# Optimization experiments

Measured on AMD Instinct MI355X. Metric: run time of the kernel, lower is better.

Reference implementation:

```python
import jax, jax.numpy as jnp
import numpy as np
import math

B, T, C, H = 8, 1024, 1024, 16
HS = C // H  # head size 64
FF = 4 * C
EPS = 1e-5


def quant_weight(W, e, b):
    """Fake-quant with straight-through rounding, per QLinear.forward.
    W:[...,out,in], e:[...,out,1], b:[...,out,1] -> effective weight 2**e * round_ste(clip(2**-e * W))."""
    b_rel = jax.nn.relu(b)
    mn = jnp.where(b_rel > 0, -(2.0 ** (b_rel - 1)), 0.0)
    mx = jnp.where(b_rel > 0, 2.0 ** (b_rel - 1) - 1.0, 0.0)
    qw = jnp.clip((2.0 ** (-e)) * W, mn, mx)
    w = qw + jax.lax.stop_gradient(jnp.round(qw) - qw)  # STE round
    return (2.0 ** e) * w


def layer_norm(x, g, beta):
    mu = jnp.mean(x, axis=-1, keepdims=True)
    var = jnp.mean((x - mu) ** 2, axis=-1, keepdims=True)
    return (x - mu) * jax.lax.rsqrt(var + EPS) * g + beta


def _uniform(key, shape, fan_in):
    s = 1.0 / math.sqrt(fan_in)
    return jax.random.uniform(key, shape, jnp.float32, -s, s)


def setup_inputs() -> dict:
    key = jax.random.key(0)
    ks = jax.random.split(key, 8)
    d = {"x": jax.random.normal(ks[0], (B, T, C), jnp.float32)}
    # stacked per-head QKV QLinear params (bias=False)
    d["Wq"] = _uniform(ks[1], (H, HS, C), C)
    d["Wk"] = _uniform(ks[2], (H, HS, C), C)
    d["Wv"] = _uniform(ks[3], (H, HS, C), C)
    for n in ("q", "k", "v"):
        d["e" + n] = jnp.full((H, HS, 1), -8.0, jnp.float32)
        d["b" + n] = jnp.full((H, HS, 1), 32.0, jnp.float32)
    # output projection QLinear (bias=True)
    d["Wp"] = _uniform(ks[4], (C, C), C)
    d["ep"] = jnp.full((C, 1), -8.0, jnp.float32)
    d["bp"] = jnp.full((C, 1), 32.0, jnp.float32)
    d["biasp"] = jnp.zeros((C,), jnp.float32)
    # FFN QLinears
    d["W1"] = _uniform(ks[5], (FF, C), C)
    d["e1"] = jnp.full((FF, 1), -8.0, jnp.float32)
    d["b1"] = jnp.full((FF, 1), 32.0, jnp.float32)
    d["bias1"] = jnp.zeros((FF,), jnp.float32)
    d["W2"] = _uniform(ks[6], (C, FF), FF)
    d["e2"] = jnp.full((C, 1), -8.0, jnp.float32)
    d["b2"] = jnp.full((C, 1), 32.0, jnp.float32)
    d["bias2"] = jnp.zeros((C,), jnp.float32)
    # LayerNorms
    d["g1"] = jnp.ones((C,), jnp.float32)
    d["be1"] = jnp.zeros((C,), jnp.float32)
    d["g2"] = jnp.ones((C,), jnp.float32)
    d["be2"] = jnp.zeros((C,), jnp.float32)
    return d


def block_forward(x, Wq, eq, bq, Wk, ek, bk, Wv, ev, bv,
                  Wp, ep, bp, biasp, W1, e1, b1, bias1, W2, e2, b2, bias2,
                  g1, be1, g2, be2):
    h = layer_norm(x, g1, be1)
    q = jnp.einsum('btc,hdc->bhtd', h, quant_weight(Wq, eq, bq))
    k = jnp.einsum('btc,hdc->bhtd', h, quant_weight(Wk, ek, bk))
    v = jnp.einsum('btc,hdc->bhtd', h, quant_weight(Wv, ev, bv))
    # NOTE: source scales by C**-0.5 where C = n_embd (not head_size)
    wei = jnp.einsum('bhtd,bhsd->bhts', q, k) * (C ** -0.5)
    causal = jnp.tril(jnp.ones((T, T), bool))
    wei = jnp.where(causal, wei, -jnp.inf)
    wei = jax.nn.softmax(wei, axis=-1)
    att = jnp.einsum('bhts,bhsd->bhtd', wei, v)  # [B,H,T,HS]
    att = att.transpose(0, 2, 1, 3).reshape(B, T, C)  # concat heads
    x = x + att @ quant_weight(Wp, ep, bp).T + biasp
    h2 = layer_norm(x, g2, be2)
    f = jax.nn.relu(h2 @ quant_weight(W1, e1, b1).T + bias1)
    f = f @ quant_weight(W2, e2, b2).T + bias2
    return x + f


def reference(x, Wq, eq, bq, Wk, ek, bk, Wv, ev, bv,
              Wp, ep, bp, biasp, W1, e1, b1, bias1, W2, e2, b2, bias2,
              g1, be1, g2, be2):
    return block_forward(x, Wq, eq, bq, Wk, ek, bk, Wv, ev, bv,
                         Wp, ep, bp, biasp, W1, e1, b1, bias1, W2, e2, b2, bias2,
                         g1, be1, g2, be2)
```

## Files before the change

### kernel.cpp

```cpp
#include <hip/hip_runtime.h>
#include <hip/hip_bf16.h>
#include <math.h>

#define DEVI __device__ __forceinline__

typedef __attribute__((ext_vector_type(8))) short bf16x8;
typedef __attribute__((ext_vector_type(4))) float f32x4;

DEVI unsigned short f2bf(float f) {
    union { float f; unsigned u; } v; v.f = f;
    unsigned r = v.u + 0x7FFFu + ((v.u >> 16) & 1u);
    return (unsigned short)(r >> 16);
}

DEVI float bf2f(unsigned short u) {
    union { unsigned u; float f; } v; v.u = (unsigned)u << 16; return v.f;
}

DEVI unsigned cvtpk(float lo, float hi) {
    unsigned d;
    asm volatile("v_cvt_pk_bf16_f32 %0, %1, %2" : "=v"(d) : "v"(lo), "v"(hi));
    return d;
}

DEVI void gload16(const void* g, void* l) {
    __builtin_amdgcn_global_load_lds((const __attribute__((address_space(1))) void*)g,
                                     (__attribute__((address_space(3))) void*)l, 16, 0, 0);
}

#define WAITVM4() asm volatile("s_waitcnt vmcnt(4)" ::: "memory")
#define WAITVM0() asm volatile("s_waitcnt vmcnt(0)" ::: "memory")
#define WAITLG0() asm volatile("s_waitcnt lgkmcnt(0)" ::: "memory")
#define WAITLG8() asm volatile("s_waitcnt lgkmcnt(8)" ::: "memory")
#define BAR()     __builtin_amdgcn_s_barrier()
#define SB()      __builtin_amdgcn_sched_barrier(0)

__global__ __launch_bounds__(256) void fused_pre_kernel(
    const float* __restrict__ Wq, const float* __restrict__ Wk, const float* __restrict__ Wv,
    const float* __restrict__ Wp, const float* __restrict__ W1, const float* __restrict__ W2,
    const float* __restrict__ eq, const float* __restrict__ ek, const float* __restrict__ ev,
    const float* __restrict__ ep, const float* __restrict__ e1, const float* __restrict__ e2,
    const float* __restrict__ bq, const float* __restrict__ bk, const float* __restrict__ bv,
    const float* __restrict__ bp, const float* __restrict__ b1, const float* __restrict__ b2,
    unsigned short* __restrict__ Wqkvq, unsigned short* __restrict__ Wpq,
    unsigned short* __restrict__ W1q, unsigned short* __restrict__ W2q,
    const float* __restrict__ x, const float* __restrict__ g1, const float* __restrict__ be1,
    unsigned short* __restrict__ hbuf)
{
    const int M1 = 1 << 20;
    if (blockIdx.x < 2048) {
        const int NCH = 3 * M1;
        const int STRIDE = 2048 * 256;
        for (int c = blockIdx.x * blockDim.x + threadIdx.x; c < NCH; c += STRIDE) {
            int elem = c * 4;
            const float *W, *e, *b; unsigned short* o; int lgK, local;
            if (elem < M1)            { W = Wq; e = eq; b = bq; o = Wqkvq;          lgK = 10; local = elem; }
            else if (elem < 2 * M1)   { W = Wk; e = ek; b = bk; o = Wqkvq + M1;     lgK = 10; local = elem - M1; }
            else if (elem < 3 * M1)   { W = Wv; e = ev; b = bv; o = Wqkvq + 2 * M1; lgK = 10; local = elem - 2 * M1; }
            else if (elem < 4 * M1)   { W = Wp; e = ep; b = bp; o = Wpq;            lgK = 10; local = elem - 3 * M1; }
            else if (elem < 8 * M1)   { W = W1; e = e1; b = b1; o = W1q;            lgK = 10; local = elem - 4 * M1; }
            else                      { W = W2; e = e2; b = b2; o = W2q;            lgK = 12; local = elem - 8 * M1; }
            int row = local >> lgK;
            float evv = e[row], bvv = b[row];
            float br = fmaxf(bvv, 0.f);
            float mn, mx;
            if (br > 0.f) { float p = exp2f(br - 1.f); mn = -p; mx = p - 1.f; }
            else          { mn = 0.f; mx = 0.f; }
            float si = exp2f(-evv), so = exp2f(evv);
            union { float4 v4; float a[4]; } v;
            v.v4 = *(const float4*)(W + local);
            union { unsigned short u[4]; unsigned long long ll; } ot;
            #pragma unroll
            for (int j = 0; j < 4; j++) {
                float qw = fminf(fmaxf(si * v.a[j], mn), mx);
                ot.u[j] = f2bf(so * rintf(qw));
            }
            *(unsigned long long*)(o + local) = ot.ll;
        }
    } else {
        int row = (blockIdx.x - 2048) * 4 + (threadIdx.x >> 6);
        int lane = threadIdx.x & 63;
        const float* xp = x + (size_t)row * 1024 + lane * 16;
        float a[16];
        #pragma unroll
        for (int j = 0; j < 4; j++) {
            float4 v = *(const float4*)(xp + j * 4);
            a[j * 4] = v.x; a[j * 4 + 1] = v.y; a[j * 4 + 2] = v.z; a[j * 4 + 3] = v.w;
        }
        float s = 0.f, s2 = 0.f;
        #pragma unroll
        for (int i = 0; i < 16; i++) { s += a[i]; s2 += a[i] * a[i]; }
        #pragma unroll
        for (int off = 1; off < 64; off <<= 1) { s += __shfl_xor(s, off); s2 += __shfl_xor(s2, off); }
        float mu = s * (1.0f / 1024.0f);
        float var = s2 * (1.0f / 1024.0f) - mu * mu;
        float rs = rsqrtf(var + 1e-5f);
        int c0 = lane * 16;
        float r[16];
        #pragma unroll
        for (int i = 0; i < 16; i++) r[i] = (a[i] - mu) * rs * g1[c0 + i] + be1[c0 + i];
        unsigned w[8];
        #pragma unroll
        for (int j = 0; j < 8; j++) w[j] = cvtpk(r[2 * j], r[2 * j + 1]);
        unsigned short* op = hbuf + (size_t)row * 1024 + c0;
        *(uint4*)(op)     = *(uint4*)&w[0];
        *(uint4*)(op + 8) = *(uint4*)&w[4];
    }
}

__global__ __launch_bounds__(256) void ln_bf_kernel(
    const unsigned short* __restrict__ xb, const float* __restrict__ g, const float* __restrict__ be,
    unsigned short* __restrict__ out)
{
    int row = blockIdx.x * 4 + (threadIdx.x >> 6);
    int lane = threadIdx.x & 63;
    const unsigned short* xp = xb + (size_t)row * 1024 + lane * 16;
    float a[16];
    #pragma unroll
    for (int j = 0; j < 2; j++) {
        bf16x8 v = *(const bf16x8*)(xp + j * 8);
        #pragma unroll
        for (int i = 0; i < 8; i++) a[j * 8 + i] = bf2f(((unsigned short*)&v)[i]);
    }
    float s = 0.f, s2 = 0.f;
    #pragma unroll
    for (int i = 0; i < 16; i++) { s += a[i]; s2 += a[i] * a[i]; }
    #pragma unroll
    for (int off = 1; off < 64; off <<= 1) { s += __shfl_xor(s, off); s2 += __shfl_xor(s2, off); }
    float mu = s * (1.0f / 1024.0f);
    float var = s2 * (1.0f / 1024.0f) - mu * mu;
    float rs = rsqrtf(var + 1e-5f);
    int c0 = lane * 16;
    float r[16];
    #pragma unroll
    for (int i = 0; i < 16; i++) r[i] = (a[i] - mu) * rs * g[c0 + i] + be[c0 + i];
    unsigned w[8];
    #pragma unroll
    for (int j = 0; j < 8; j++) w[j] = cvtpk(r[2 * j], r[2 * j + 1]);
    unsigned short* op = out + (size_t)row * 1024 + c0;
    *(uint4*)(op)     = *(uint4*)&w[0];
    *(uint4*)(op + 8) = *(uint4*)&w[4];
}

#define GSTAGE(buf, kt) do { \
    _Pragma("unroll") for (int q_ = 0; q_ < 2; q_++) { \
        int idx_ = q_ * 512 + tid; int row_ = idx_ >> 3; int gs_ = (idx_ & 7) ^ (row_ & 7); \
        gload16(A  + (size_t)(brow + row_) * K + (kt) * 64 + gs_ * 8, &As[buf][idx_ * 8]); \
        gload16(Bw + (size_t)(bcol + row_) * K + (kt) * 64 + gs_ * 8, &Bs[buf][idx_ * 8]); \
    } } while (0)

template<int EP>
__global__ __launch_bounds__(512, 2) void gemm_bt(
    const unsigned short* __restrict__ A, const unsigned short* __restrict__ Bw,
    int N, int K,
    const float* __restrict__ bias, const float* __restrict__ res,
    const unsigned short* __restrict__ resb,
    float* __restrict__ outf, unsigned short* __restrict__ outb)
{
    __shared__ __align__(16) unsigned short As[2][128 * 64];
    __shared__ __align__(16) unsigned short Bs[2][128 * 64];
    int tid = threadIdx.x, lane = tid & 63, wave = tid >> 6;
    int gx = gridDim.x;
    int nwg = gx * gridDim.y;
    int id = blockIdx.y * gx + blockIdx.x;
    int swz = (id & 7) * (nwg >> 3) + (id >> 3);
    int brow = (swz / gx) * 128, bcol = (swz % gx) * 128;
    int wr = wave >> 2, wc = wave & 3;
    int r = lane & 15, g4 = lane >> 4;
    f32x4 acc[4][2];
    #pragma unroll
    for (int i = 0; i < 4; i++)
        #pragma unroll
        for (int j = 0; j < 2; j++) acc[i][j] = (f32x4){0.f, 0.f, 0.f, 0.f};

    int nt = K >> 6;
    GSTAGE(0, 0);
    __syncthreads();
    int cur = 0;
    for (int t = 0; t < nt; ++t) {
        if (t + 1 < nt) { GSTAGE(cur ^ 1, t + 1); WAITVM4(); }
        else            { WAITVM0(); }
        __builtin_amdgcn_s_barrier();
        #pragma unroll
        for (int kk = 0; kk < 2; kk++) {
            bf16x8 af[4], bfr[2];
            #pragma unroll
            for (int mi = 0; mi < 4; mi++) {
                int rh = wr * 64 + mi * 16 + r;
                af[mi] = *(const bf16x8*)&As[cur][rh * 64 + (((kk * 4 + g4) ^ (rh & 7)) << 3)];
            }
            #pragma unroll
            for (int ni = 0; ni < 2; ni++) {
                int rh = wc * 32 + ni * 16 + r;
                bfr[ni] = *(const bf16x8*)&Bs[cur][rh * 64 + (((kk * 4 + g4) ^ (rh & 7)) << 3)];
            }
            #pragma unroll
            for (int mi = 0; mi < 4; mi++)
                #pragma unroll
                for (int ni = 0; ni < 2; ni++)
                    acc[mi][ni] = __builtin_amdgcn_mfma_f32_16x16x32_bf16(af[mi], bfr[ni], acc[mi][ni], 0, 0, 0);
        }
        __builtin_amdgcn_s_barrier();
        cur ^= 1;
    }

    #pragma unroll
    for (int mi = 0; mi < 4; mi++)
        #pragma unroll
        for (int ni = 0; ni < 2; ni++)
            #pragma unroll
            for (int i = 0; i < 4; i++) {
                int row = brow + wr * 64 + mi * 16 + g4 * 4 + i;
                int col = bcol + wc * 32 + ni * 16 + r;
                float v = acc[mi][ni][i];
                if (EP == 0) {
                    outb[(size_t)row * N + col] = f2bf(v);
                } else if (EP == 1) {
                    outf[(size_t)row * N + col] = v + bias[col] + res[(size_t)row * N + col];
                } else if (EP == 2) {
                    outb[(size_t)row * N + col] = f2bf(fmaxf(v + bias[col], 0.f));
                } else if (EP == 3) {
                    outb[(size_t)row * N + col] = f2bf(v + bias[col] + res[(size_t)row * N + col]);
                } else {
                    outf[(size_t)row * N + col] = v + bias[col] + bf2f(resb[(size_t)row * N + col]);
                }
            }
}

#define STAGE_A(b, h, kt) do { \
    _Pragma("unroll") \
    for (int ld = 0; ld < 2; ld++) { \
        int idx = ld * 512 + tid; int rw = idx >> 3; int gs = (idx & 7) ^ (rw & 7); \
        gload16(Aa + (size_t)(brow + (h) * 128 + rw) * K + (kt) * 64 + gs * 8, &As[b][h][idx * 8]); \
    } } while (0)

#define STAGE_B(b, h, kt) do { \
    _Pragma("unroll") \
    for (int ld = 0; ld < 2; ld++) { \
        int idx = ld * 512 + tid; int rw = idx >> 3; int gs = (idx & 7) ^ (rw & 7); \
        gload16(Bw + (size_t)(bcol + (h) * 128 + rw) * K + (kt) * 64 + gs * 8, &Bs[b][h][idx * 8]); \
    } } while (0)

#define RD_A(b, mh) do { \
    _Pragma("unroll") for (int mi = 0; mi < 4; mi++) \
    _Pragma("unroll") for (int kk = 0; kk < 2; kk++) { \
        int rh = (mh) * 64 + mi * 16 + r; \
        af[mi][kk] = *(const bf16x8*)&As[b][wr][rh * 64 + (((kk * 4 + g4) ^ (rh & 7)) << 3)]; \
    } } while (0)

#define RD_B2(b, nh) do { \
    _Pragma("unroll") for (int nj = 0; nj < 2; nj++) \
    _Pragma("unroll") for (int kk = 0; kk < 2; kk++) { \
        int rh = (wc & 1) * 64 + ((nh) * 2 + nj) * 16 + r; \
        bfr[(nh) * 2 + nj][kk] = *(const bf16x8*)&Bs[b][wc >> 1][rh * 64 + (((kk * 4 + g4) ^ (rh & 7)) << 3)]; \
    } } while (0)

#define QUAD(mh, nh) do { \
    __builtin_amdgcn_s_setprio(1); \
    _Pragma("unroll") for (int mi = 0; mi < 4; mi++) \
    _Pragma("unroll") for (int nj = 0; nj < 2; nj++) \
    _Pragma("unroll") for (int kk = 0; kk < 2; kk++) \
        acc[(mh) * 4 + mi][(nh) * 2 + nj] = __builtin_amdgcn_mfma_f32_16x16x32_bf16( \
            af[mi][kk], bfr[(nh) * 2 + nj][kk], acc[(mh) * 4 + mi][(nh) * 2 + nj], 0, 0, 0); \
    __builtin_amdgcn_s_setprio(0); \
    } while (0)

template<int EP>
__global__ __launch_bounds__(512, 2) void gemm256(
    const unsigned short* __restrict__ Aa, const unsigned short* __restrict__ Bw,
    int N, int K,
    const float* __restrict__ bias, const float* __restrict__ res,
    float* __restrict__ outf, unsigned short* __restrict__ outb)
{
    __shared__ __align__(16) unsigned short As[2][2][128 * 64];
    __shared__ __align__(16) unsigned short Bs[2][2][128 * 64];
    int tid = threadIdx.x, lane = tid & 63, wave = tid >> 6;
    int gx = gridDim.x;
    int nwg = gx * gridDim.y;
    int id = blockIdx.y * gx + blockIdx.x;
    int swz = (id & 7) * (nwg >> 3) + (id >> 3);
    int brow = (swz / gx) * 256, bcol = (swz % gx) * 256;
    int wr = wave >> 2, wc = wave & 3;
    int r = lane & 15, g4 = lane >> 4;
    int KT = K >> 6;

    f32x4 acc[8][4];
    #pragma unroll
    for (int i = 0; i < 8; i++)
        #pragma unroll
        for (int j = 0; j < 4; j++) acc[i][j] = (f32x4){0.f, 0.f, 0.f, 0.f};
    bf16x8 af[4][2], bfr[4][2];

    STAGE_A(0, 0, 0); STAGE_A(0, 1, 0); STAGE_B(0, 0, 0); STAGE_B(0, 1, 0);
    STAGE_B(1, 0, 1); STAGE_B(1, 1, 1);
    WAITVM4();
    BAR();

    for (int t = 0; t < KT; t += 2) {
        RD_A(0, 0); RD_B2(0, 0);
        STAGE_A(1, 0, t + 1);
        WAITLG8();
        BAR(); WAITLG0(); SB();
        QUAD(0, 0);
        BAR();
        RD_B2(0, 1);
        STAGE_A(1, 1, t + 1);
        BAR(); WAITLG0(); SB();
        QUAD(0, 1);
        BAR();
        RD_A(0, 1);
        if (t + 2 < KT) STAGE_B(0, 0, t + 2);
        BAR(); WAITLG0(); SB();
        QUAD(1, 1);
        BAR();
        if (t + 2 < KT) { STAGE_B(0, 1, t + 2); WAITVM4(); } else { WAITVM0(); }
        BAR(); WAITLG0(); SB();
        QUAD(1, 0);
        BAR();
        RD_A(1, 0); RD_B2(1, 0);
        if (t + 2 < KT) STAGE_A(0, 0, t + 2);
        WAITLG8();
        BAR(); WAITLG0(); SB();
        QUAD(0, 0);
        BAR();
        RD_B2(1, 1);
        if (t + 2 < KT) STAGE_A(0, 1, t + 2);
        BAR(); WAITLG0(); SB();
        QUAD(0, 1);
        BAR();
        RD_A(1, 1);
        if (t + 3 < KT) STAGE_B(1, 0, t + 3);
        BAR(); WAITLG0(); SB();
        QUAD(1, 1);
        BAR();
        if (t + 3 < KT) { STAGE_B(1, 1, t + 3); WAITVM4(); } else { WAITVM0(); }
        BAR(); WAITLG0(); SB();
        QUAD(1, 0);
        BAR();
    }

    #pragma unroll
    for (int m = 0; m < 8; m++)
        #pragma unroll
        for (int n = 0; n < 4; n++)
            #pragma unroll
            for (int j = 0; j < 4; j++) {
                int row = brow + wr * 128 + m * 16 + g4 * 4 + j;
                int col = bcol + wc * 64 + n * 16 + r;
                float v = acc[m][n][j];
                if (EP == 0) {
                    outb[(size_t)row * N + col] = f2bf(v);
                } else if (EP == 1) {
                    outf[(size_t)row * N + col] = v + bias[col] + res[(size_t)row * N + col];
                } else {
                    outb[(size_t)row * N + col] = f2bf(fmaxf(v + bias[col], 0.f));
                }
            }
}

__global__ __launch_bounds__(512, 4) void attn_kernel(
    const unsigned short* __restrict__ qkv, unsigned short* __restrict__ att)
{
    __shared__ __align__(16) unsigned short Ks[2][64 * 64];
    __shared__ __align__(16) unsigned short Vt[2][64 * 66];
    __shared__ __align__(16) unsigned short Ps[2][64 * 64];
    int tid = threadIdx.x, lane = tid & 63, w = tid >> 6;
    int half = w >> 2;
    int pi = blockIdx.x;
    int bh = blockIdx.y, bb = bh >> 4, hh = bh & 15;
    int r = lane & 15, g4 = lane >> 4;
    const unsigned short* base = qkv + (size_t)bb * 1024 * 3072;
    const float SCL = 0.03125f * 1.4426950408889634f;
    int vd = tid & 63, vsb = tid >> 6;
    int prow = (w & 3) * 16 + r;
    int pswz = (r & 7) << 3;

    for (int sidx = 0; sidx < 2; sidx++) {
        int s = sidx ? (7 - pi) : pi;
        int qt = 2 * s + half;
        int qtmax = 2 * s + 1;
        int qrow = qt * 64 + prow;

        bf16x8 qf[2];
        #pragma unroll
        for (int kk = 0; kk < 2; kk++)
            qf[kk] = *(const bf16x8*)&base[(size_t)qrow * 3072 + hh * 64 + kk * 32 + g4 * 8];

        f32x4 oacc[4];
        #pragma unroll
        for (int i = 0; i < 4; i++) oacc[i] = (f32x4){0.f, 0.f, 0.f, 0.f};
        float m_i = -INFINITY, l_i = 0.f;

        unsigned short vtmp[8];
        {
            int row = tid >> 3, slot = tid & 7;
            int gs = slot ^ (row & 7);
            gload16(base + (size_t)row * 3072 + 1024 + hh * 64 + gs * 8, &Ks[0][tid * 8]);
            #pragma unroll
            for (int i2 = 0; i2 < 8; i2++)
                vtmp[i2] = base[(size_t)(vsb * 8 + i2) * 3072 + 2048 + hh * 64 + vd];
            union { unsigned short u[8]; bf16x8 v; } w0;
            #pragma unroll
            for (int i2 = 0; i2 < 8; i2++) w0.u[i2] = vtmp[i2];
            *(bf16x8*)&Vt[0][vd * 66 + (vsb ^ (vd & 7)) * 8] = w0.v;
        }
        __syncthreads();

        for (int ki = 0; ki <= qtmax; ki++) {
            int cur = ki & 1;
            bool pre = (ki < qtmax);
            bool act = (ki <= qt);
            if (pre) {
                int k1 = (ki + 1) * 64;
                int row = tid >> 3, slot = tid & 7;
                int gs = slot ^ (row & 7);
                gload16(base + (size_t)(k1 + row) * 3072 + 1024 + hh * 64 + gs * 8, &Ks[cur ^ 1][tid * 8]);
                #pragma unroll
                for (int i2 = 0; i2 < 8; i2++)
                    vtmp[i2] = base[(size_t)(k1 + vsb * 8 + i2) * 3072 + 2048 + hh * 64 + vd];
            }

            if (act) {
                int k0 = ki * 64;
                f32x4 sacc[4];
                #pragma unroll
                for (int c4 = 0; c4 < 4; c4++) sacc[c4] = (f32x4){0.f, 0.f, 0.f, 0.f};
                #pragma unroll
                for (int c4 = 0; c4 < 4; c4++) {
                    int krow = c4 * 16 + r;
                    #pragma unroll
                    for (int kk = 0; kk < 2; kk++) {
                        int slot = (g4 + kk * 4) ^ (krow & 7);
                        bf16x8 kf = *(const bf16x8*)&Ks[cur][krow * 64 + slot * 8];
                        sacc[c4] = __builtin_amdgcn_mfma_f32_16x16x32_bf16(kf, qf[kk], sacc[c4], 0, 0, 0);
                    }
                }
                bool diag = (ki == qt);
                float sv[4][4];
                float smax = -INFINITY;
                #pragma unroll
                for (int c4 = 0; c4 < 4; c4++)
                    #pragma unroll
                    for (int i = 0; i < 4; i++) {
                        float sa = sacc[c4][i];
                        if (diag && (k0 + c4 * 16 + g4 * 4 + i) > qrow) sa = -INFINITY;
                        sv[c4][i] = sa;
                        smax = fmaxf(smax, sa);
                    }
                smax = fmaxf(smax, __shfl_xor(smax, 16));
                smax = fmaxf(smax, __shfl_xor(smax, 32));
                if (!__all((smax - m_i) * SCL <= 8.f)) {
                    float mn = fmaxf(m_i, smax);
                    float fs = exp2f((m_i - mn) * SCL);
                    m_i = mn;
                    l_i *= fs;
                    #pragma unroll
                    for (int n4 = 0; n4 < 4; n4++)
                        #pragma unroll
                        for (int i = 0; i < 4; i++) oacc[n4][i] *= fs;
                }
                float nb = -m_i * SCL;
                float rsum = 0.f;
                float pv[4][4];
                #pragma unroll
                for (int c4 = 0; c4 < 4; c4++)
                    #pragma unroll
                    for (int i = 0; i < 4; i++) {
                        float p = exp2f(fmaf(sv[c4][i], SCL, nb));
                        pv[c4][i] = p;
                        rsum += p;
                    }
                rsum += __shfl_xor(rsum, 16);
                rsum += __shfl_xor(rsum, 32);
                l_i += rsum;
                #pragma unroll
                for (int c4 = 0; c4 < 4; c4++) {
                    unsigned long long ll = (unsigned long long)cvtpk(pv[c4][0], pv[c4][1])
                                          | ((unsigned long long)cvtpk(pv[c4][2], pv[c4][3]) << 32);
                    *(unsigned long long*)&Ps[half][(prow * 64 + c4 * 16 + g4 * 4) ^ pswz] = ll;
                }
                WAITLG0();
            }
            if (pre) {
                union { unsigned short u[8]; bf16x8 v; } w0;
                #pragma unroll
                for (int i2 = 0; i2 < 8; i2++) w0.u[i2] = vtmp[i2];
                *(bf16x8*)&Vt[cur ^ 1][vd * 66 + (vsb ^ (vd & 7)) * 8] = w0.v;
            }
            if (act) {
                bf16x8 pa[2];
                #pragma unroll
                for (int kk = 0; kk < 2; kk++)
                    pa[kk] = *(const bf16x8*)&Ps[half][(prow * 64 + kk * 32 + g4 * 8) ^ pswz];
                #pragma unroll
                for (int n4 = 0; n4 < 4; n4++) {
                    int d = n4 * 16 + r;
                    #pragma unroll
                    for (int kk = 0; kk < 2; kk++) {
                        bf16x8 vf = *(const bf16x8*)&Vt[cur][d * 66 + (((kk * 4 + g4) ^ (d & 7)) << 3)];
                        oacc[n4] = __builtin_amdgcn_mfma_f32_16x16x32_bf16(vf, pa[kk], oacc[n4], 0, 0, 0);
                    }
                }
            }
            __syncthreads();
        }

        float inv = 1.f / l_i;
        #pragma unroll
        for (int n4 = 0; n4 < 4; n4++) {
            unsigned long long ll = (unsigned long long)cvtpk(oacc[n4][0] * inv, oacc[n4][1] * inv)
                                  | ((unsigned long long)cvtpk(oacc[n4][2] * inv, oacc[n4][3] * inv) << 32);
            size_t oidx = ((size_t)(bb * 1024 + qrow)) * 1024 + hh * 64 + n4 * 16 + g4 * 4;
            *(unsigned long long*)&att[oidx] = ll;
        }
    }
}

extern "C" void kernel_launch(void* const* d_in, const int* in_sizes, int n_in,
                              void* d_out, int out_size, void* d_ws, size_t ws_size,
                              hipStream_t stream)
{
    const float* x     = (const float*)d_in[0];
    const float* Wq    = (const float*)d_in[1];
    const float* Wk    = (const float*)d_in[2];
    const float* Wv    = (const float*)d_in[3];
    const float* eq    = (const float*)d_in[4];
    const float* bq    = (const float*)d_in[5];
    const float* ek    = (const float*)d_in[6];
    const float* bk    = (const float*)d_in[7];
    const float* ev    = (const float*)d_in[8];
    const float* bv    = (const float*)d_in[9];
    const float* Wp    = (const float*)d_in[10];
    const float* ep    = (const float*)d_in[11];
    const float* bp    = (const float*)d_in[12];
    const float* biasp = (const float*)d_in[13];
    const float* W1    = (const float*)d_in[14];
    const float* e1    = (const float*)d_in[15];
    const float* b1    = (const float*)d_in[16];
    const float* bias1 = (const float*)d_in[17];
    const float* W2    = (const float*)d_in[18];
    const float* e2    = (const float*)d_in[19];
    const float* b2    = (const float*)d_in[20];
    const float* bias2 = (const float*)d_in[21];
    const float* g1    = (const float*)d_in[22];
    const float* be1   = (const float*)d_in[23];
    const float* g2    = (const float*)d_in[24];
    const float* be2   = (const float*)d_in[25];

    const size_t MB = 1ull << 20;
    char* ws = (char*)d_ws;
    unsigned short* Wqkvq = (unsigned short*)(ws);
    unsigned short* Wpq   = (unsigned short*)(ws + 6 * MB);
    unsigned short* W1q   = (unsigned short*)(ws + 8 * MB);
    unsigned short* W2q   = (unsigned short*)(ws + 16 * MB);
    unsigned short* hbuf  = (unsigned short*)(ws + 24 * MB);
    unsigned short* qkvb  = (unsigned short*)(ws + 40 * MB);
    unsigned short* fbuf  = qkvb;
    unsigned short* attb  = (unsigned short*)(ws + 88 * MB);
    unsigned short* x2b   = (unsigned short*)(ws + 104 * MB);

    fused_pre_kernel<<<4096, 256, 0, stream>>>(Wq, Wk, Wv, Wp, W1, W2,
                                               eq, ek, ev, ep, e1, e2,
                                               bq, bk, bv, bp, b1, b2,
                                               Wqkvq, Wpq, W1q, W2q,
                                               x, g1, be1, hbuf);

    gemm_bt<0><<<dim3(24, 64), 512, 0, stream>>>(hbuf, Wqkvq, 3072, 1024, nullptr, nullptr, nullptr, nullptr, qkvb);
    attn_kernel<<<dim3(4, 128), 512, 0, stream>>>(qkvb, attb);
    gemm_bt<3><<<dim3(8, 64), 512, 0, stream>>>(attb, Wpq, 1024, 1024, biasp, x, nullptr, nullptr, x2b);
    ln_bf_kernel<<<2048, 256, 0, stream>>>(x2b, g2, be2, hbuf);
    gemm256<2><<<dim3(16, 32), 512, 0, stream>>>(hbuf, W1q, 4096, 1024, bias1, nullptr, nullptr, fbuf);
    gemm_bt<4><<<dim3(8, 64), 512, 0, stream>>>(fbuf, W2q, 1024, 4096, bias2, nullptr, x2b, (float*)d_out, nullptr);
}
```

Measured before the change: 318.7 us.

## Replace 256-tile FFN1 GEMM with 128-tile kernel and add 4-wave GEMM variant

```diff
diff --git a/kernel.cpp b/kernel.cpp
--- a/kernel.cpp
+++ b/kernel.cpp
@@ -28,12 +28,11 @@
                                      (__attribute__((address_space(3))) void*)l, 16, 0, 0);
 }
 
+#define WAITVM8() asm volatile("s_waitcnt vmcnt(8)" ::: "memory")
 #define WAITVM4() asm volatile("s_waitcnt vmcnt(4)" ::: "memory")
 #define WAITVM0() asm volatile("s_waitcnt vmcnt(0)" ::: "memory")
 #define WAITLG0() asm volatile("s_waitcnt lgkmcnt(0)" ::: "memory")
-#define WAITLG8() asm volatile("s_waitcnt lgkmcnt(8)" ::: "memory")
 #define BAR()     __builtin_amdgcn_s_barrier()
-#define SB()      __builtin_amdgcn_sched_barrier(0)
 
 __global__ __launch_bounds__(256) void fused_pre_kernel(
     const float* __restrict__ Wq, const float* __restrict__ Wk, const float* __restrict__ Wv,
@@ -142,7 +141,7 @@
     *(uint4*)(op + 8) = *(uint4*)&w[4];
 }
 
-#define GSTAGE(buf, kt) do { \
+#define GSTAGE8(buf, kt) do { \
     _Pragma("unroll") for (int q_ = 0; q_ < 2; q_++) { \
         int idx_ = q_ * 512 + tid; int row_ = idx_ >> 3; int gs_ = (idx_ & 7) ^ (row_ & 7); \
         gload16(A  + (size_t)(brow + row_) * K + (kt) * 64 + gs_ * 8, &As[buf][idx_ * 8]); \
@@ -174,11 +173,11 @@
         for (int j = 0; j < 2; j++) acc[i][j] = (f32x4){0.f, 0.f, 0.f, 0.f};
 
     int nt = K >> 6;
-    GSTAGE(0, 0);
+    GSTAGE8(0, 0);
     __syncthreads();
     int cur = 0;
     for (int t = 0; t < nt; ++t) {
-        if (t + 1 < nt) { GSTAGE(cur ^ 1, t + 1); WAITVM4(); }
+        if (t + 1 < nt) { GSTAGE8(cur ^ 1, t + 1); WAITVM4(); }
         else            { WAITVM0(); }
         __builtin_amdgcn_s_barrier();
         #pragma unroll
@@ -227,133 +226,87 @@
             }
 }
 
-#define STAGE_A(b, h, kt) do { \
-    _Pragma("unroll") \
-    for (int ld = 0; ld < 2; ld++) { \
-        int idx = ld * 512 + tid; int rw = idx >> 3; int gs = (idx & 7) ^ (rw & 7); \
-        gload16(Aa + (size_t)(brow + (h) * 128 + rw) * K + (kt) * 64 + gs * 8, &As[b][h][idx * 8]); \
+#define GSTAGE4(buf, kt) do { \
+    _Pragma("unroll") for (int q_ = 0; q_ < 4; q_++) { \
+        int idx_ = q_ * 256 + tid; int row_ = idx_ >> 3; int gs_ = (idx_ & 7) ^ (row_ & 7); \
+        gload16(A  + (size_t)(brow + row_) * K + (kt) * 64 + gs_ * 8, &As[buf][idx_ * 8]); \
+        gload16(Bw + (size_t)(bcol + row_) * K + (kt) * 64 + gs_ * 8, &Bs[buf][idx_ * 8]); \
     } } while (0)
 
-#define STAGE_B(b, h, kt) do { \
-    _Pragma("unroll") \
-    for (int ld = 0; ld < 2; ld++) { \
-        int idx = ld * 512 + tid; int rw = idx >> 3; int gs = (idx & 7) ^ (rw & 7); \
-        gload16(Bw + (size_t)(bcol + (h) * 128 + rw) * K + (kt) * 64 + gs * 8, &Bs[b][h][idx * 8]); \
-    } } while (0)
-
-#define RD_A(b, mh) do { \
-    _Pragma("unroll") for (int mi = 0; mi < 4; mi++) \
-    _Pragma("unroll") for (int kk = 0; kk < 2; kk++) { \
-        int rh = (mh) * 64 + mi * 16 + r; \
-        af[mi][kk] = *(const bf16x8*)&As[b][wr][rh * 64 + (((kk * 4 + g4) ^ (rh & 7)) << 3)]; \
-    } } while (0)
-
-#define RD_B2(b, nh) do { \
-    _Pragma("unroll") for (int nj = 0; nj < 2; nj++) \
-    _Pragma("unroll") for (int kk = 0; kk < 2; kk++) { \
-        int rh = (wc & 1) * 64 + ((nh) * 2 + nj) * 16 + r; \
-        bfr[(nh) * 2 + nj][kk] = *(const bf16x8*)&Bs[b][wc >> 1][rh * 64 + (((kk * 4 + g4) ^ (rh & 7)) << 3)]; \
-    } } while (0)
-
-#define QUAD(mh, nh) do { \
-    __builtin_amdgcn_s_setprio(1); \
-    _Pragma("unroll") for (int mi = 0; mi < 4; mi++) \
-    _Pragma("unroll") for (int nj = 0; nj < 2; nj++) \
-    _Pragma("unroll") for (int kk = 0; kk < 2; kk++) \
-        acc[(mh) * 4 + mi][(nh) * 2 + nj] = __builtin_amdgcn_mfma_f32_16x16x32_bf16( \
-            af[mi][kk], bfr[(nh) * 2 + nj][kk], acc[(mh) * 4 + mi][(nh) * 2 + nj], 0, 0, 0); \
-    __builtin_amdgcn_s_setprio(0); \
-    } while (0)
-
 template<int EP>
-__global__ __launch_bounds__(512, 2) void gemm256(
-    const unsigned short* __restrict__ Aa, const unsigned short* __restrict__ Bw,
+__global__ __launch_bounds__(256) void gemm_bt4(
+    const unsigned short* __restrict__ A, const unsigned short* __restrict__ Bw,
     int N, int K,
     const float* __restrict__ bias, const float* __restrict__ res,
+    const unsigned short* __restrict__ resb,
     float* __restrict__ outf, unsigned short* __restrict__ outb)
 {
-    __shared__ __align__(16) unsigned short As[2][2][128 * 64];
-    __shared__ __align__(16) unsigned short Bs[2][2][128 * 64];
+    __shared__ __align__(16) unsigned short As[2][128 * 64];
+    __shared__ __align__(16) unsigned short Bs[2][128 * 64];
     int tid = threadIdx.x, lane = tid & 63, wave = tid >> 6;
     int gx = gridDim.x;
     int nwg = gx * gridDim.y;
     int id = blockIdx.y * gx + blockIdx.x;
     int swz = (id & 7) * (nwg >> 3) + (id >> 3);
-    int brow = (swz / gx) * 256, bcol = (swz % gx) * 256;
-    int wr = wave >> 2, wc = wave & 3;
+    int brow = (swz / gx) * 128, bcol = (swz % gx) * 128;
+    int wr = wave >> 1, wc = wave & 1;
     int r = lane & 15, g4 = lane >> 4;
-    int KT = K >> 6;
-
-    f32x4 acc[8][4];
-    #pragma unroll
-    for (int i = 0; i < 8; i++)
+    f32x4 acc[4][4];
+    #pragma unroll
+    for (int i = 0; i < 4; i++)
         #pragma unroll
         for (int j = 0; j < 4; j++) acc[i][j] = (f32x4){0.f, 0.f, 0.f, 0.f};
-    bf16x8 af[4][2], bfr[4][2];
-
-    STAGE_A(0, 0, 0); STAGE_A(0, 1, 0); STAGE_B(0, 0, 0); STAGE_B(0, 1, 0);
-    STAGE_B(1, 0, 1); STAGE_B(1, 1, 1);
-    WAITVM4();
-    BAR();
-
-    for (int t = 0; t < KT; t += 2) {
-        RD_A(0, 0); RD_B2(0, 0);
-        STAGE_A(1, 0, t + 1);
-        WAITLG8();
-        BAR(); WAITLG0(); SB();
-        QUAD(0, 0);
-        BAR();
-        RD_B2(0, 1);
-        STAGE_A(1, 1, t + 1);
-        BAR(); WAITLG0(); SB();
-        QUAD(0, 1);
-        BAR();
-        RD_A(0, 1);
-        if (t + 2 < KT) STAGE_B(0, 0, t + 2);
-        BAR(); WAITLG0(); SB();
-        QUAD(1, 1);
-        BAR();
-        if (t + 2 < KT) { STAGE_B(0, 1, t + 2); WAITVM4(); } else { WAITVM0(); }
-        BAR(); WAITLG0(); SB();
-        QUAD(1, 0);
-        BAR();
-        RD_A(1, 0); RD_B2(1, 0);
-        if (t + 2 < KT) STAGE_A(0, 0, t + 2);
-        WAITLG8();
-        BAR(); WAITLG0(); SB();
-        QUAD(0, 0);
-        BAR();
-        RD_B2(1, 1);
-        if (t + 2 < KT) STAGE_A(0, 1, t + 2);
-        BAR(); WAITLG0(); SB();
-        QUAD(0, 1);
-        BAR();
-        RD_A(1, 1);
-        if (t + 3 < KT) STAGE_B(1, 0, t + 3);
-        BAR(); WAITLG0(); SB();
-        QUAD(1, 1);
-        BAR();
-        if (t + 3 < KT) { STAGE_B(1, 1, t + 3); WAITVM4(); } else { WAITVM0(); }
-        BAR(); WAITLG0(); SB();
-        QUAD(1, 0);
-        BAR();
+
+    int nt = K >> 6;
+    GSTAGE4(0, 0);
+    __syncthreads();
+    int cur = 0;
+    for (int t = 0; t < nt; ++t) {
+        if (t + 1 < nt) { GSTAGE4(cur ^ 1, t + 1); WAITVM8(); }
+        else            { WAITVM0(); }
+        __builtin_amdgcn_s_barrier();
+        #pragma unroll
+        for (int kk = 0; kk < 2; kk++) {
+            bf16x8 af[4], bfr[4];
+            #pragma unroll
+            for (int mi = 0; mi < 4; mi++) {
+                int rh = wr * 64 + mi * 16 + r;
+                af[mi] = *(const bf16x8*)&As[cur][rh * 64 + (((kk * 4 + g4) ^ (rh & 7)) << 3)];
+            }
+            #pragma unroll
+            for (int ni = 0; ni < 4; ni++) {
+                int rh = wc * 64 + ni * 16 + r;
+                bfr[ni] = *(const bf16x8*)&Bs[cur][rh * 64 + (((kk * 4 + g4) ^ (rh & 7)) << 3)];
+            }
+            #pragma unroll
+            for (int mi = 0; mi < 4; mi++)
+                #pragma unroll
+                for (int ni = 0; ni < 4; ni++)
+                    acc[mi][ni] = __builtin_amdgcn_mfma_f32_16x16x32_bf16(af[mi], bfr[ni], acc[mi][ni], 0, 0, 0);
+        }
+        __builtin_amdgcn_s_barrier();
+        cur ^= 1;
     }
 
     #pragma unroll
-    for (int m = 0; m < 8; m++)
-        #pragma unroll
-        for (int n = 0; n < 4; n++)
-            #pragma unroll
-            for (int j = 0; j < 4; j++) {
-                int row = brow + wr * 128 + m * 16 + g4 * 4 + j;
-                int col = bcol + wc * 64 + n * 16 + r;
-                float v = acc[m][n][j];
+    for (int mi = 0; mi < 4; mi++)
+        #pragma unroll
+        for (int ni = 0; ni < 4; ni++)
+            #pragma unroll
+            for (int i = 0; i < 4; i++) {
+                int row = brow + wr * 64 + mi * 16 + g4 * 4 + i;
+                int col = bcol + wc * 64 + ni * 16 + r;
+                float v = acc[mi][ni][i];
                 if (EP == 0) {
                     outb[(size_t)row * N + col] = f2bf(v);
                 } else if (EP == 1) {
                     outf[(size_t)row * N + col] = v + bias[col] + res[(size_t)row * N + col];
+                } else if (EP == 2) {
+                    outb[(size_t)row * N + col] = f2bf(fmaxf(v + bias[col], 0.f));
+                } else if (EP == 3) {
+                    outb[(size_t)row * N + col] = f2bf(v + bias[col] + res[(size_t)row * N + col]);
                 } else {
-                    outb[(size_t)row * N + col] = f2bf(fmaxf(v + bias[col], 0.f));
+                    outf[(size_t)row * N + col] = v + bias[col] + bf2f(resb[(size_t)row * N + col]);
                 }
             }
 }
@@ -567,8 +520,8 @@
 
     gemm_bt<0><<<dim3(24, 64), 512, 0, stream>>>(hbuf, Wqkvq, 3072, 1024, nullptr, nullptr, nullptr, nullptr, qkvb);
     attn_kernel<<<dim3(4, 128), 512, 0, stream>>>(qkvb, attb);
-    gemm_bt<3><<<dim3(8, 64), 512, 0, stream>>>(attb, Wpq, 1024, 1024, biasp, x, nullptr, nullptr, x2b);
+    gemm_bt4<3><<<dim3(8, 64), 256, 0, stream>>>(attb, Wpq, 1024, 1024, biasp, x, nullptr, nullptr, x2b);
     ln_bf_kernel<<<2048, 256, 0, stream>>>(x2b, g2, be2, hbuf);
-    gemm256<2><<<dim3(16, 32), 512, 0, stream>>>(hbuf, W1q, 4096, 1024, bias1, nullptr, nullptr, fbuf);
-    gemm_bt<4><<<dim3(8, 64), 512, 0, stream>>>(fbuf, W2q, 1024, 4096, bias2, nullptr, x2b, (float*)d_out, nullptr);
-}
+    gemm_bt<2><<<dim3(32, 64), 512, 0, stream>>>(hbuf, W1q, 4096, 1024, bias1, nullptr, nullptr, nullptr, fbuf);
+    gemm_bt4<4><<<dim3(8, 64), 256, 0, stream>>>(fbuf, W2q, 1024, 4096, bias2, nullptr, x2b, (float*)d_out, nullptr);
+}
```

After: 329.8 us. 1.03x slower.
